# Optimization experiments

Hardware: AMD Instinct MI355X
Metric: run time of the kernel (lower is better)

Reference implementation:

```python
import jax, jax.numpy as jnp
import numpy as np
from functools import partial

BETA = 0.9
THR = 1.0
NUM_STEPS = 50
SLOPE = 15.0
BN_EPS = 1e-5
NHID = 250
NCLS = 10

@jax.custom_vjp
def spike_fn(x):
    return (x > 0).astype(x.dtype)

def _spike_fwd(x):
    return spike_fn(x), x

def _spike_bwd(x, g):
    # snntorch fast_sigmoid surrogate: grad = 1 / (slope*|x| + 1)^2
    return (g / (SLOPE * jnp.abs(x) + 1.0) ** 2,)

spike_fn.defvjp(_spike_fwd, _spike_bwd)

def conv1d(x, w, b, stride=1):
    # x: [B,C,L], w: [O,I,K]
    y = jax.lax.conv_general_dilated(x, w, (stride,), 'VALID',
                                     dimension_numbers=('NCH', 'OIH', 'NCH'))
    return y + b[None, :, None]

def bn_eval(x, g, b, m, v):
    inv = g / jnp.sqrt(v + BN_EPS)
    return (x - m[None, :, None]) * inv[None, :, None] + b[None, :, None]

def lif_step(mem, cur):
    # snntorch Leaky (reset_mechanism='subtract'): reset uses detached spike of previous mem
    reset = jax.lax.stop_gradient((mem > THR).astype(mem.dtype))
    mem = BETA * mem + cur - reset * THR
    spk = spike_fn(mem - THR)
    return mem, spk

def maxpool4(x):
    # MaxPool1d(4) on [B,C,L]
    return jax.lax.reduce_window(x, -jnp.inf, jax.lax.max, (1, 1, 4), (1, 1, 4), 'VALID')

def get_embedding(x, c1w, c1b, bn1g, bn1b, bn1m, bn1v, c2w, c2b, bn2g, bn2b, bn2m, bn2v,
                  fc1w, fc1b, fcsw, fcsb):
    B = x.shape[0]
    # input-invariant part of the per-step loop (conv1+BN1 on x)
    cur1 = bn_eval(conv1d(x, c1w, c1b, stride=4), bn1g, bn1b, bn1m, bn1v)  # [B,16,1981]

    def step(carry, _):
        mem1, mem2, mem3 = carry
        mem1, spk1 = lif_step(mem1, cur1)
        pooled = maxpool4(spk1)                                   # [B,16,495]
        cur2 = bn_eval(conv1d(pooled, c2w, c2b), bn2g, bn2b, bn2m, bn2v)  # [B,32,493]
        mem2, spk2 = lif_step(mem2, cur2)
        flat = spk2.reshape(B, -1)                                # [B,15776]
        cur3 = flat @ fc1w.T + fc1b                               # dropout is eval -> identity
        mem3, spk3 = lif_step(mem3, cur3)
        return (mem1, mem2, mem3), spk3

    carry0 = (jnp.zeros_like(cur1),
              jnp.zeros((B, 32, 493), cur1.dtype),
              jnp.zeros((B, NHID), cur1.dtype))
    _, spk_rec = jax.lax.scan(step, carry0, None, length=NUM_STEPS)  # [T,B,250]

    firing_rate = spk_rec.sum(axis=0)                                 # [B,250]
    latency = jnp.argmax(spk_rec, axis=0).astype(x.dtype) / NUM_STEPS # first-spike idx
    comb = jnp.concatenate([firing_rate, latency], axis=1)            # [B,500]
    out = comb @ fcsw.T + fcsb                                        # [B,128]
    norm = jnp.maximum(jnp.linalg.norm(out, axis=1, keepdims=True), 1e-12)
    return out / norm

def setup_inputs() -> dict:
    key = jax.random.key(0)
    ks = jax.random.split(key, 16)
    B, L = 32, 8000
    d = {}
    d['x1'] = jax.random.normal(ks[0], (B, 1, L), jnp.float32)
    d['x2'] = jax.random.normal(ks[1], (B, 1, L), jnp.float32)
    d['c1w'] = jax.random.normal(ks[2], (16, 1, 80), jnp.float32) * 0.1
    d['c1b'] = jax.random.normal(ks[3], (16,), jnp.float32) * 0.1
    d['bn1g'] = jnp.ones((16,), jnp.float32)
    d['bn1b'] = jnp.zeros((16,), jnp.float32)
    d['bn1m'] = jax.random.normal(ks[4], (16,), jnp.float32) * 0.1
    d['bn1v'] = jax.random.uniform(ks[5], (16,), jnp.float32, 0.5, 1.5)
    d['c2w'] = jax.random.normal(ks[6], (32, 16, 3), jnp.float32) * 0.1
    d['c2b'] = jax.random.normal(ks[7], (32,), jnp.float32) * 0.1
    d['bn2g'] = jnp.ones((32,), jnp.float32)
    d['bn2b'] = jnp.zeros((32,), jnp.float32)
    d['bn2m'] = jax.random.normal(ks[8], (32,), jnp.float32) * 0.1
    d['bn2v'] = jax.random.uniform(ks[9], (32,), jnp.float32, 0.5, 1.5)
    d['fc1w'] = jax.random.normal(ks[10], (NHID, 15776), jnp.float32) * 0.02
    d['fc1b'] = jax.random.normal(ks[11], (NHID,), jnp.float32) * 0.02
    d['fcsw'] = jax.random.normal(ks[12], (128, 2 * NHID), jnp.float32) * 0.05
    d['fcsb'] = jax.random.normal(ks[13], (128,), jnp.float32) * 0.05
    return d

def reference(x1, x2, c1w, c1b, bn1g, bn1b, bn1m, bn1v, c2w, c2b, bn2g, bn2b, bn2m, bn2v,
              fc1w, fc1b, fcsw, fcsb):
    params = (c1w, c1b, bn1g, bn1b, bn1m, bn1v, c2w, c2b, bn2g, bn2b, bn2m, bn2v,
              fc1w, fc1b, fcsw, fcsb)
    emb1 = get_embedding(x1, *params)
    emb2 = get_embedding(x2, *params)
    return (emb1, emb2)
```

## Files before the change

### kernel.cpp

```cpp
#include <hip/hip_runtime.h>
#include <math.h>
#include <stdint.h>

#define BETA 0.9f
#define THR 1.0f
#define T_STEPS 50
#define BN_EPS 1e-5f

#define NITEM 64
#define C1 16
#define L1 1981
#define L1P 1984
#define P4 495
#define C2 32
#define L2 493
#define L2PAD 496
#define KTOT 15872
#define KREAL 15776
#define NFC 250
#define NPAD 256
#define KSPLIT 16
#define KRANGE 992
#define KSTEPS 31
#define NKTILE 496
#define MROWS 3200
#define TSLICE 1015808

#define OFF_CUR1 0UL
#define OFF_POOL 8126464UL
#define OFF_SPK2 34340864UL
#define OFF_WT   85131264UL
#define OFF_PART 101384192UL
#define OFF_COMB 127598592UL
#define OFF_CUR3 16384UL

typedef __attribute__((ext_vector_type(8))) short bf16x8;
typedef __attribute__((ext_vector_type(4))) float f32x4;

__device__ __forceinline__ uint32_t f32_to_bf16_rne(float f) {
  uint32_t u = __float_as_uint(f);
  return (u + 0x7FFFu + ((u >> 16) & 1u)) >> 16;
}

__device__ __forceinline__ bf16x8 frag_from_bytes(uint2 a) {
  union { uint32_t u[4]; bf16x8 v; } c;
  c.u[0] = (a.x & 0x00010001u) * 0x3F80u;
  c.u[1] = ((a.x >> 8) & 0x00010001u) * 0x3F80u;
  c.u[2] = (a.y & 0x00010001u) * 0x3F80u;
  c.u[3] = ((a.y >> 8) & 0x00010001u) * 0x3F80u;
  return c.v;
}

__global__ __launch_bounds__(256) void k_wt(const float* __restrict__ fc1w,
                                            uint8_t* __restrict__ wTf) {
  __shared__ float ftile[256][33];
  int kt = blockIdx.x;
  int tid = threadIdx.x;
  {
    int kk = tid & 31;
    int r8 = tid >> 5;
    int k = kt * 32 + kk;
    int oc = k / L2PAD;
    int pos = k - oc * L2PAD;
    bool kvalid = (pos < L2);
    size_t src = (size_t)oc * L2 + pos;
#pragma unroll
    for (int p = 0; p < 32; ++p) {
      int n = p * 8 + r8;
      float w = 0.f;
      if (kvalid && n < NFC) w = fc1w[(size_t)n * KREAL + src];
      ftile[n][kk] = w;
    }
  }
  __syncthreads();
  int n = tid;
  int wv = n >> 6, ni = (n >> 4) & 3, r16 = n & 15;
  uint32_t h16[32], l16[32];
#pragma unroll
  for (int kl = 0; kl < 32; ++kl) {
    float w = ftile[n][kl];
    uint32_t hb = f32_to_bf16_rne(w);
    float hf = __uint_as_float(hb << 16);
    h16[kl] = hb;
    l16[kl] = f32_to_bf16_rne(w - hf);
  }
  uint8_t* tb = wTf + (size_t)kt * 32768 + wv * 8192 + ni * 2048;
#pragma unroll
  for (int g = 0; g < 4; ++g) {
    int b = g * 8;
    uint4 h;
    h.x = h16[b + 0] | (h16[b + 2] << 16);
    h.y = h16[b + 1] | (h16[b + 3] << 16);
    h.z = h16[b + 4] | (h16[b + 6] << 16);
    h.w = h16[b + 5] | (h16[b + 7] << 16);
    *reinterpret_cast<uint4*>(tb + (g * 16 + r16) * 16) = h;
    uint4 l;
    l.x = l16[b + 0] | (l16[b + 2] << 16);
    l.y = l16[b + 1] | (l16[b + 3] << 16);
    l.z = l16[b + 4] | (l16[b + 6] << 16);
    l.w = l16[b + 5] | (l16[b + 7] << 16);
    *reinterpret_cast<uint4*>(tb + 1024 + (g * 16 + r16) * 16) = l;
  }
}

__global__ __launch_bounds__(256) void k_conv1(const float* __restrict__ x1, const float* __restrict__ x2,
                                               const float* __restrict__ c1w, const float* __restrict__ c1b,
                                               const float* __restrict__ g, const float* __restrict__ bb,
                                               const float* __restrict__ mn, const float* __restrict__ vr,
                                               float* __restrict__ cur1) {
  __shared__ __align__(16) float xs[1104];
  int item = blockIdx.y;
  int pc = blockIdx.x;
  int tid = threadIdx.x;
  const float* x = (item < 32 ? x1 : x2) + (item & 31) * 8000;
  int xoff = pc * 1024;
  for (int i = tid; i < 1100; i += 256) {
    int gi = xoff + i;
    xs[i] = (gi < 8000) ? x[gi] : 0.f;
  }
  __syncthreads();
  int p = pc * 256 + tid;
  bool pv = (p < L1);
  const float4* xs4 = reinterpret_cast<const float4*>(xs);
  for (int c = 0; c < C1; ++c) {
    float s = g[c] / sqrtf(vr[c] + BN_EPS);
    float sh = (c1b[c] - mn[c]) * s + bb[c];
    const float4* w4 = reinterpret_cast<const float4*>(c1w + c * 80);
    float acc = 0.f;
#pragma unroll
    for (int k4 = 0; k4 < 20; ++k4) {
      float4 wv4 = w4[k4];
      float4 xv = xs4[tid + k4];
      acc += wv4.x * xv.x; acc += wv4.y * xv.y;
      acc += wv4.z * xv.z; acc += wv4.w * xv.w;
    }
    if (pv) cur1[(item * C1 + c) * L1P + p] = acc * s + sh;
  }
}

__global__ __launch_bounds__(256) void k_lif1(const float* __restrict__ cur1,
                                              uint8_t* __restrict__ pooledT) {
  int item = blockIdx.y;
  int g = threadIdx.x & 3;
  int p4 = blockIdx.x * 64 + (threadIdx.x >> 2);
  if (p4 >= P4) return;
  float4 cv[4];
#pragma unroll
  for (int j = 0; j < 4; ++j)
    cv[j] = *reinterpret_cast<const float4*>(cur1 + ((size_t)item * C1 + g * 4 + j) * L1P + 4 * p4);
  float m[4][4];
#pragma unroll
  for (int j = 0; j < 4; ++j)
#pragma unroll
    for (int r = 0; r < 4; ++r) m[j][r] = 0.f;
  uint32_t* out = reinterpret_cast<uint32_t*>(pooledT + ((size_t)item * 50 * 512 + p4) * 16 + g * 4);
  for (int t = 0; t < T_STEPS; ++t) {
    uint32_t pk = 0;
#pragma unroll
    for (int j = 0; j < 4; ++j) {
      int s = 0;
#pragma unroll
      for (int r = 0; r < 4; ++r) {
        float rst = (m[j][r] > THR) ? 1.f : 0.f;
        float cvv = (r == 0) ? cv[j].x : (r == 1) ? cv[j].y : (r == 2) ? cv[j].z : cv[j].w;
        m[j][r] = BETA * m[j][r] + cvv - rst;
        s |= (m[j][r] > THR);
      }
      pk |= ((uint32_t)s) << (8 * j);
    }
    out[t * 2048] = pk;
  }
}

__global__ __launch_bounds__(256) void k_conv2(const uint8_t* __restrict__ pooledT,
                                               const float* __restrict__ c2w, const float* __restrict__ c2b,
                                               const float* __restrict__ g, const float* __restrict__ bb,
                                               const float* __restrict__ mn, const float* __restrict__ vr,
                                               uint32_t* __restrict__ spk2) {
  int item = blockIdx.y;
  int pt = blockIdx.x;
  int tid = threadIdx.x;
  int lane = tid & 63, wv = tid >> 6;
  int r16 = lane & 15, kg = lane >> 4;
  bf16x8 bw[2][2][2];
  float sh[2];
#pragma unroll
  for (int nt = 0; nt < 2; ++nt) {
    int oc = nt * 16 + r16;
    float s2 = g[oc] * rsqrtf(vr[oc] + BN_EPS);
    sh[nt] = (c2b[oc] - mn[oc]) * s2 + bb[oc];
#pragma unroll
    for (int kt = 0; kt < 2; ++kt) {
      uint32_t h[8], l[8];
#pragma unroll
      for (int j = 0; j < 8; ++j) {
        int k = kt * 32 + kg * 8 + j;
        int tap = k >> 4, ic = k & 15;
        float raw = (tap < 3) ? c2w[oc * 48 + ic * 3 + tap] * s2 : 0.f;
        uint32_t hb = f32_to_bf16_rne(raw);
        float hf = __uint_as_float(hb << 16);
        h[j] = hb;
        l[j] = f32_to_bf16_rne(raw - hf);
      }
      union { uint32_t u[4]; bf16x8 v; } ch_, cl_;
      ch_.u[0] = h[0] | (h[2] << 16); ch_.u[1] = h[1] | (h[3] << 16);
      ch_.u[2] = h[4] | (h[6] << 16); ch_.u[3] = h[5] | (h[7] << 16);
      cl_.u[0] = l[0] | (l[2] << 16); cl_.u[1] = l[1] | (l[3] << 16);
      cl_.u[2] = l[4] | (l[6] << 16); cl_.u[3] = l[5] | (l[7] << 16);
      bw[nt][kt][0] = ch_.v;
      bw[nt][kt][1] = cl_.v;
    }
  }
  const uint8_t* base = pooledT + (size_t)item * 50 * 8192;
  int rowA = pt * 64 + wv * 16 + r16;
  size_t off0 = (size_t)(rowA + (kg >> 1)) * 16 + 8 * (kg & 1);
  size_t off1 = (size_t)(rowA + 2) * 16 + 8 * (kg & 1);
  uint2 na0 = *reinterpret_cast<const uint2*>(base + off0);
  uint2 na1 = *reinterpret_cast<const uint2*>(base + off1);
  float mem[2][4] = {{0.f, 0.f, 0.f, 0.f}, {0.f, 0.f, 0.f, 0.f}};
  int pos_base = pt * 64 + wv * 16 + kg * 4;
  bool dostore = pos_base < L2PAD;
  int k0a = r16 * L2PAD + pos_base;
  int k0b = (16 + r16) * L2PAD + pos_base;
  uint32_t sidx0 = (uint32_t)(k0a >> 5) * 512u + (uint32_t)item * 8u + ((uint32_t)(k0a >> 2) & 7u);
  uint32_t sidx1 = (uint32_t)(k0b >> 5) * 512u + (uint32_t)item * 8u + ((uint32_t)(k0b >> 2) & 7u);
  for (int t = 0; t < T_STEPS; ++t) {
    uint2 a0 = na0, a1 = na1;
    const uint8_t* nb = base + (size_t)((t + 1 < T_STEPS) ? t + 1 : t) * 8192;
    na0 = *reinterpret_cast<const uint2*>(nb + off0);
    na1 = *reinterpret_cast<const uint2*>(nb + off1);
    bf16x8 af0 = frag_from_bytes(a0);
    bf16x8 af1 = frag_from_bytes(a1);
    uint32_t st[2];
#pragma unroll
    for (int nt = 0; nt < 2; ++nt) {
      f32x4 acc = (f32x4){0.f, 0.f, 0.f, 0.f};
      acc = __builtin_amdgcn_mfma_f32_16x16x32_bf16(af0, bw[nt][0][0], acc, 0, 0, 0);
      acc = __builtin_amdgcn_mfma_f32_16x16x32_bf16(af1, bw[nt][1][0], acc, 0, 0, 0);
      acc = __builtin_amdgcn_mfma_f32_16x16x32_bf16(af0, bw[nt][0][1], acc, 0, 0, 0);
      acc = __builtin_amdgcn_mfma_f32_16x16x32_bf16(af1, bw[nt][1][1], acc, 0, 0, 0);
      uint32_t packed = 0;
#pragma unroll
      for (int r = 0; r < 4; ++r) {
        float rst = (mem[nt][r] > THR) ? 1.f : 0.f;
        mem[nt][r] = BETA * mem[nt][r] + (acc[r] + sh[nt]) - rst;
        packed |= (mem[nt][r] > THR ? 1u : 0u) << (8 * r);
      }
      st[nt] = packed;
    }
    if (dostore) {
      uint32_t tb = (uint32_t)t * (TSLICE / 4);
      spk2[tb + sidx0] = st[0];
      spk2[tb + sidx1] = st[1];
    }
  }
}

__global__ __launch_bounds__(512) void k_fc1(const uint8_t* __restrict__ spk2,
                                             const uint8_t* __restrict__ wTf,
                                             float* __restrict__ part0,
                                             float* __restrict__ part1) {
  int ks = blockIdx.x;
  int mt = blockIdx.y;
  int tid = threadIdx.x;
  int lane = tid & 63, w8 = tid >> 6;
  int wv = w8 & 3, mg = w8 >> 2;
  int r16 = lane & 15, kg = lane >> 4;
  int t = mt * 2 + mg;

  f32x4 acc[4][4];
#pragma unroll
  for (int mi = 0; mi < 4; ++mi)
#pragma unroll
    for (int ni = 0; ni < 4; ++ni) acc[mi][ni] = (f32x4){0.f, 0.f, 0.f, 0.f};

  const uint8_t* abase = spk2 + (size_t)t * TSLICE + (size_t)(ks * KSTEPS) * 2048 + r16 * 32 + kg * 8;
  const uint8_t* bbase = wTf + (size_t)ks * KSTEPS * 32768 + wv * 8192 + lane * 16;

  for (int ch = 0; ch < KSTEPS; ++ch) {
    uint2 a[4];
#pragma unroll
    for (int mi = 0; mi < 4; ++mi)
      a[mi] = *reinterpret_cast<const uint2*>(abase + (size_t)ch * 2048 + mi * 512);
    bf16x8 bfr[4][2];
#pragma unroll
    for (int ni = 0; ni < 4; ++ni)
#pragma unroll
      for (int sel = 0; sel < 2; ++sel)
        bfr[ni][sel] = *reinterpret_cast<const bf16x8*>(bbase + (size_t)ch * 32768 + ni * 2048 + sel * 1024);
    bf16x8 af[4];
#pragma unroll
    for (int mi = 0; mi < 4; ++mi) af[mi] = frag_from_bytes(a[mi]);
#pragma unroll
    for (int ni = 0; ni < 4; ++ni)
#pragma unroll
      for (int mi = 0; mi < 4; ++mi) {
        acc[mi][ni] = __builtin_amdgcn_mfma_f32_16x16x32_bf16(af[mi], bfr[ni][0], acc[mi][ni], 0, 0, 0);
        acc[mi][ni] = __builtin_amdgcn_mfma_f32_16x16x32_bf16(af[mi], bfr[ni][1], acc[mi][ni], 0, 0, 0);
      }
  }
  float* pb = (ks < 8) ? (part0 + (size_t)ks * MROWS * NPAD)
                       : (part1 + (size_t)(ks - 8) * MROWS * NPAD);
  int colb = wv * 64 + r16;
  int rowb = t * 64 + kg * 4;
#pragma unroll
  for (int mi = 0; mi < 4; ++mi)
#pragma unroll
    for (int ni = 0; ni < 4; ++ni) {
      float* pp = pb + (size_t)(rowb + mi * 16) * NPAD + colb + ni * 16;
#pragma unroll
      for (int r = 0; r < 4; ++r) pp[r * NPAD] = acc[mi][ni][r];
    }
}

__global__ __launch_bounds__(256) void k_red(const float* __restrict__ part0,
                                             const float* __restrict__ part1,
                                             float* __restrict__ cur3) {
  int i = blockIdx.x * 256 + threadIdx.x;
  float s = 0.f;
#pragma unroll
  for (int ksx = 0; ksx < 8; ++ksx) s += part0[(size_t)ksx * MROWS * NPAD + i];
#pragma unroll
  for (int ksx = 0; ksx < 8; ++ksx) s += part1[(size_t)ksx * MROWS * NPAD + i];
  cur3[i] = s;
}

__global__ __launch_bounds__(256) void k_lif3(const float* __restrict__ cur3,
                                              const float* __restrict__ fc1b,
                                              float* __restrict__ comb) {
  int item = blockIdx.x;
  int n = threadIdx.x;
  if (n >= NFC) return;
  float bias = fc1b[n];
  float sv[T_STEPS];
#pragma unroll
  for (int t = 0; t < T_STEPS; ++t)
    sv[t] = cur3[(size_t)(t * NITEM + item) * NPAD + n];
  float mem = 0.f, cnt = 0.f;
  int first = -1;
#pragma unroll
  for (int t = 0; t < T_STEPS; ++t) {
    float r = (mem > THR) ? 1.f : 0.f;
    mem = BETA * mem + (bias + sv[t]) - r;
    if (mem > THR) { cnt += 1.f; if (first < 0) first = t; }
  }
  comb[item * 500 + n] = cnt;
  comb[item * 500 + NFC + n] = (first < 0) ? 0.f : ((float)first / (float)T_STEPS);
}

__global__ __launch_bounds__(128) void k_head(const float* __restrict__ comb,
                                              const float* __restrict__ fcsw,
                                              const float* __restrict__ fcsb,
                                              float* __restrict__ dout) {
  __shared__ float cr[500];
  __shared__ float red[2];
  int item = blockIdx.x;
  int o = threadIdx.x;
  for (int i = o; i < 500; i += 128) cr[i] = comb[item * 500 + i];
  __syncthreads();
  float acc = fcsb[o];
  for (int j = 0; j < 500; ++j) acc += cr[j] * fcsw[o * 500 + j];
  float sq = acc * acc;
  for (int off = 32; off > 0; off >>= 1) sq += __shfl_down(sq, off, 64);
  if ((o & 63) == 0) red[o >> 6] = sq;
  __syncthreads();
  float norm = sqrtf(red[0] + red[1]);
  norm = fmaxf(norm, 1e-12f);
  dout[item * 128 + o] = acc / norm;
}

extern "C" void kernel_launch(void* const* d_in, const int* in_sizes, int n_in,
                              void* d_out, int out_size, void* d_ws, size_t ws_size,
                              hipStream_t stream) {
  const float* x1   = (const float*)d_in[0];
  const float* x2   = (const float*)d_in[1];
  const float* c1w  = (const float*)d_in[2];
  const float* c1b  = (const float*)d_in[3];
  const float* bn1g = (const float*)d_in[4];
  const float* bn1b = (const float*)d_in[5];
  const float* bn1m = (const float*)d_in[6];
  const float* bn1v = (const float*)d_in[7];
  const float* c2w  = (const float*)d_in[8];
  const float* c2b  = (const float*)d_in[9];
  const float* bn2g = (const float*)d_in[10];
  const float* bn2b = (const float*)d_in[11];
  const float* bn2m = (const float*)d_in[12];
  const float* bn2v = (const float*)d_in[13];
  const float* fc1w = (const float*)d_in[14];
  const float* fc1b = (const float*)d_in[15];
  const float* fcsw = (const float*)d_in[16];
  const float* fcsb = (const float*)d_in[17];

  char* ws = (char*)d_ws;
  float*    cur1    = (float*)(ws + OFF_CUR1);
  float*    cur3    = (float*)(ws + OFF_CUR1 + OFF_CUR3);
  uint8_t*  pooledT = (uint8_t*)(ws + OFF_POOL);
  float*    part1   = (float*)(ws + OFF_POOL);
  uint8_t*  spk2    = (uint8_t*)(ws + OFF_SPK2);
  uint8_t*  wTf     = (uint8_t*)(ws + OFF_WT);
  float*    part0   = (float*)(ws + OFF_PART);
  float*    comb    = (float*)(ws + OFF_COMB);

  k_wt<<<dim3(NKTILE), dim3(256), 0, stream>>>(fc1w, wTf);
  k_conv1<<<dim3(8, NITEM), dim3(256), 0, stream>>>(x1, x2, c1w, c1b, bn1g, bn1b, bn1m, bn1v, cur1);
  k_lif1<<<dim3(8, NITEM), dim3(256), 0, stream>>>(cur1, pooledT);
  k_conv2<<<dim3(8, NITEM), dim3(256), 0, stream>>>(pooledT, c2w, c2b, bn2g, bn2b, bn2m, bn2v,
                                                    (uint32_t*)spk2);
  k_fc1<<<dim3(KSPLIT, T_STEPS / 2), dim3(512), 0, stream>>>(spk2, wTf, part0, part1);
  k_red<<<dim3(MROWS * NPAD / 256), dim3(256), 0, stream>>>(part0, part1, cur3);
  k_lif3<<<dim3(NITEM), dim3(256), 0, stream>>>(cur3, fc1b, comb);
  k_head<<<dim3(NITEM), dim3(128), 0, stream>>>(comb, fcsw, fcsb, (float*)d_out);
}
```

Baseline: 198.1 us.

## Fuse conv1 with LIF1 through shared memory and transpose head weights

Merges the conv1+BN kernel with the first LIF/maxpool kernel, so the conv output stays in shared memory and no longer makes a global round trip or needs its own launch. Adds a small kernel that transposes the head weights so the head matvec reads them coalesced, and unrolls that loop. It also moves the comb buffer to a new workspace offset. The cost is one extra tiny launch and more shared memory per block in the fused kernel.

```diff
diff --git a/kernel.cpp b/kernel.cpp
--- a/kernel.cpp
+++ b/kernel.cpp
@@ -10,7 +10,6 @@
 #define NITEM 64
 #define C1 16
 #define L1 1981
-#define L1P 1984
 #define P4 495
 #define C2 32
 #define L2 493
@@ -33,6 +32,8 @@
 #define OFF_PART 101384192UL
 #define OFF_COMB 127598592UL
 #define OFF_CUR3 16384UL
+#define OFF_COMB2 4194304UL
+#define OFF_FCSWT 6291456UL
 
 typedef __attribute__((ext_vector_type(8))) short bf16x8;
 typedef __attribute__((ext_vector_type(4))) float f32x4;
@@ -103,12 +104,22 @@
   }
 }
 
-__global__ __launch_bounds__(256) void k_conv1(const float* __restrict__ x1, const float* __restrict__ x2,
-                                               const float* __restrict__ c1w, const float* __restrict__ c1b,
-                                               const float* __restrict__ g, const float* __restrict__ bb,
-                                               const float* __restrict__ mn, const float* __restrict__ vr,
-                                               float* __restrict__ cur1) {
+__global__ __launch_bounds__(256) void k_wh(const float* __restrict__ fcsw,
+                                            float* __restrict__ fcswT) {
+  int i = blockIdx.x * 256 + threadIdx.x;
+  if (i < 64000) {
+    int j = i >> 7, o = i & 127;
+    fcswT[i] = fcsw[o * 500 + j];
+  }
+}
+
+__global__ __launch_bounds__(256) void k_conv1l1(const float* __restrict__ x1, const float* __restrict__ x2,
+                                                 const float* __restrict__ c1w, const float* __restrict__ c1b,
+                                                 const float* __restrict__ g, const float* __restrict__ bb,
+                                                 const float* __restrict__ mn, const float* __restrict__ vr,
+                                                 uint8_t* __restrict__ pooledT) {
   __shared__ __align__(16) float xs[1104];
+  __shared__ __align__(16) float cur_l[16][260];
   int item = blockIdx.y;
   int pc = blockIdx.x;
   int tid = threadIdx.x;
@@ -119,8 +130,6 @@
     xs[i] = (gi < 8000) ? x[gi] : 0.f;
   }
   __syncthreads();
-  int p = pc * 256 + tid;
-  bool pv = (p < L1);
   const float4* xs4 = reinterpret_cast<const float4*>(xs);
   for (int c = 0; c < C1; ++c) {
     float s = g[c] / sqrtf(vr[c] + BN_EPS);
@@ -134,26 +143,23 @@
       acc += wv4.x * xv.x; acc += wv4.y * xv.y;
       acc += wv4.z * xv.z; acc += wv4.w * xv.w;
     }
-    if (pv) cur1[(item * C1 + c) * L1P + p] = acc * s + sh;
-  }
-}
-
-__global__ __launch_bounds__(256) void k_lif1(const float* __restrict__ cur1,
-                                              uint8_t* __restrict__ pooledT) {
-  int item = blockIdx.y;
-  int g = threadIdx.x & 3;
-  int p4 = blockIdx.x * 64 + (threadIdx.x >> 2);
+    cur_l[c][tid] = acc * s + sh;
+  }
+  __syncthreads();
+  int gq = tid & 3;
+  int p4l = tid >> 2;
+  int p4 = pc * 64 + p4l;
   if (p4 >= P4) return;
   float4 cv[4];
 #pragma unroll
   for (int j = 0; j < 4; ++j)
-    cv[j] = *reinterpret_cast<const float4*>(cur1 + ((size_t)item * C1 + g * 4 + j) * L1P + 4 * p4);
+    cv[j] = *reinterpret_cast<const float4*>(&cur_l[gq * 4 + j][4 * p4l]);
   float m[4][4];
 #pragma unroll
   for (int j = 0; j < 4; ++j)
 #pragma unroll
     for (int r = 0; r < 4; ++r) m[j][r] = 0.f;
-  uint32_t* out = reinterpret_cast<uint32_t*>(pooledT + ((size_t)item * 50 * 512 + p4) * 16 + g * 4);
+  uint32_t* out = reinterpret_cast<uint32_t*>(pooledT + ((size_t)item * 50 * 512 + p4) * 16 + gq * 4);
   for (int t = 0; t < T_STEPS; ++t) {
     uint32_t pk = 0;
 #pragma unroll
@@ -349,7 +355,7 @@
 }
 
 __global__ __launch_bounds__(128) void k_head(const float* __restrict__ comb,
-                                              const float* __restrict__ fcsw,
+                                              const float* __restrict__ fcswT,
                                               const float* __restrict__ fcsb,
                                               float* __restrict__ dout) {
   __shared__ float cr[500];
@@ -359,7 +365,8 @@
   for (int i = o; i < 500; i += 128) cr[i] = comb[item * 500 + i];
   __syncthreads();
   float acc = fcsb[o];
-  for (int j = 0; j < 500; ++j) acc += cr[j] * fcsw[o * 500 + j];
+#pragma unroll 4
+  for (int j = 0; j < 500; ++j) acc += cr[j] * fcswT[j * 128 + o];
   float sq = acc * acc;
   for (int off = 32; off > 0; off >>= 1) sq += __shfl_down(sq, off, 64);
   if ((o & 63) == 0) red[o >> 6] = sq;
@@ -392,22 +399,23 @@
   const float* fcsb = (const float*)d_in[17];
 
   char* ws = (char*)d_ws;
-  float*    cur1    = (float*)(ws + OFF_CUR1);
   float*    cur3    = (float*)(ws + OFF_CUR1 + OFF_CUR3);
+  float*    comb    = (float*)(ws + OFF_CUR1 + OFF_COMB2);
+  float*    fcswT   = (float*)(ws + OFF_CUR1 + OFF_FCSWT);
   uint8_t*  pooledT = (uint8_t*)(ws + OFF_POOL);
   float*    part1   = (float*)(ws + OFF_POOL);
   uint8_t*  spk2    = (uint8_t*)(ws + OFF_SPK2);
   uint8_t*  wTf     = (uint8_t*)(ws + OFF_WT);
   float*    part0   = (float*)(ws + OFF_PART);
-  float*    comb    = (float*)(ws + OFF_COMB);
 
   k_wt<<<dim3(NKTILE), dim3(256), 0, stream>>>(fc1w, wTf);
-  k_conv1<<<dim3(8, NITEM), dim3(256), 0, stream>>>(x1, x2, c1w, c1b, bn1g, bn1b, bn1m, bn1v, cur1);
-  k_lif1<<<dim3(8, NITEM), dim3(256), 0, stream>>>(cur1, pooledT);
+  k_wh<<<dim3(250), dim3(256), 0, stream>>>(fcsw, fcswT);
+  k_conv1l1<<<dim3(8, NITEM), dim3(256), 0, stream>>>(x1, x2, c1w, c1b, bn1g, bn1b, bn1m, bn1v,
+                                                      pooledT);
   k_conv2<<<dim3(8, NITEM), dim3(256), 0, stream>>>(pooledT, c2w, c2b, bn2g, bn2b, bn2m, bn2v,
                                                     (uint32_t*)spk2);
   k_fc1<<<dim3(KSPLIT, T_STEPS / 2), dim3(512), 0, stream>>>(spk2, wTf, part0, part1);
   k_red<<<dim3(MROWS * NPAD / 256), dim3(256), 0, stream>>>(part0, part1, cur3);
   k_lif3<<<dim3(NITEM), dim3(256), 0, stream>>>(cur3, fc1b, comb);
-  k_head<<<dim3(NITEM), dim3(128), 0, stream>>>(comb, fcsw, fcsb, (float*)d_out);
-}
+  k_head<<<dim3(NITEM), dim3(128), 0, stream>>>(comb, fcswT, fcsb, (float*)d_out);
+}
```

Result: slower. 206.0 us (+4.0%).
